# Kernel optimization log

Measured on AMD Instinct MI355X. Metric: run time of the kernel, lower is better.

## Reference

```python
import jax, jax.numpy as jnp
import numpy as np

NUM_HEADS = 8
HEAD_DIM = 64  # hidden_dim // num_heads = 512 // 8
THRESHOLD = 0.5


def setup_inputs() -> dict:
    key = jax.random.key(0)
    ks = jax.random.split(key, 12)
    B, T, D, Hd = 4, 1024, 512, 512
    s = 0.02
    inp = {
        'x': jax.random.normal(ks[0], (B, T, D), dtype=jnp.float32),
        'Wq': jax.random.normal(ks[1], (D, Hd), dtype=jnp.float32) * s,
        'bq': jnp.zeros((Hd,), jnp.float32),
        'Wk': jax.random.normal(ks[2], (D, Hd), dtype=jnp.float32) * s,
        'bk': jnp.zeros((Hd,), jnp.float32),
        'Wv': jax.random.normal(ks[3], (D, Hd), dtype=jnp.float32) * s,
        'bv': jnp.zeros((Hd,), jnp.float32),
        'conv_w': jax.random.normal(ks[4], (NUM_HEADS,), dtype=jnp.float32) * 0.3,
        'conv_b': jnp.zeros((1,), jnp.float32),
        'Wfh': jax.random.normal(ks[5], (Hd, Hd), dtype=jnp.float32) * s,
        'bfh': jnp.zeros((Hd,), jnp.float32),
        'Wfg': jax.random.normal(ks[6], (Hd, Hd), dtype=jnp.float32) * s,
        'bfg': jnp.zeros((Hd,), jnp.float32),
        'Wrh': jax.random.normal(ks[7], (Hd, Hd), dtype=jnp.float32) * s,
        'brh': jnp.zeros((Hd,), jnp.float32),
        'Wrg': jax.random.normal(ks[8], (Hd, Hd), dtype=jnp.float32) * s,
        'brg': jnp.zeros((Hd,), jnp.float32),
    }
    return inp


def reference(x, Wq, bq, Wk, bk, Wv, bv, conv_w, conv_b,
              Wfh, bfh, Wfg, bfg, Wrh, brh, Wrg, brg):
    B, T, D = x.shape
    H, hd = NUM_HEADS, HEAD_DIM
    scale = hd ** -0.5

    q = (x @ Wq + bq).reshape(B, T, H, hd).transpose(0, 2, 1, 3)  # [B,H,T,hd]
    k = (x @ Wk + bk).reshape(B, T, H, hd).transpose(0, 2, 1, 3)
    v = (x @ Wv + bv).reshape(B, T, H, hd).transpose(0, 2, 1, 3)

    scores = jnp.einsum('bhqd,bhkd->bhqk', q, k) * scale        # [B,H,T,T]
    A_t = jax.nn.softmax(scores, axis=-1)

    # cross-head 1x1 conv: weighted sum over heads -> [B,1,T,T]
    R_f = jax.nn.sigmoid(jnp.einsum('bhqk,h->bqk', A_t, conv_w) + conv_b[0])
    R_f = R_f[:, None]                                           # [B,1,T,T]
    M_f = (R_f <= THRESHOLD).astype(A_t.dtype)
    M_r = (1.0 - R_f <= THRESHOLD).astype(A_t.dtype)

    A_f = jax.nn.softmax(A_t * M_f, axis=-1)
    A_r = jax.nn.softmax(A_t * M_r, axis=-1)

    T_f = jnp.einsum('bhqk,bhkd->bhqd', A_f, v).transpose(0, 2, 1, 3).reshape(B, T, H * hd)
    T_r = jnp.einsum('bhqk,bhkd->bhqd', A_r, v).transpose(0, 2, 1, 3).reshape(B, T, H * hd)

    F_f = T_f @ Wfh + bfh
    G_f = jax.nn.sigmoid(T_f @ Wfg + bfg)
    F_r = T_r @ Wrh + brh
    G_r = jax.nn.sigmoid(T_r @ Wrg + brg)

    G_cat = jax.nn.softmax(jnp.stack([G_f, G_r], axis=-1), axis=-1)  # [B,T,Hd,2]
    F_t = F_f * G_cat[..., 0] + F_r * G_cat[..., 1]
    return F_t
```

## Files before the change

kernel.cpp:

```cpp
#include <hip/hip_runtime.h>
#include <hip/hip_bf16.h>
#include <stdint.h>

typedef short bf16x8 __attribute__((ext_vector_type(8)));
typedef float f32x4 __attribute__((ext_vector_type(4)));

__device__ __forceinline__ unsigned short f2bf(float f) {
  union { float f; unsigned int u; } v;
  v.f = f;
  unsigned int u = v.u;
  u = (u + 0x7fffu + ((u >> 16) & 1u)) >> 16;
  return (unsigned short)u;
}

__device__ __forceinline__ unsigned int pack_bf16(float x, float y) {
  return (unsigned int)f2bf(x) | ((unsigned int)f2bf(y) << 16);
}

typedef union { bf16x8 v; unsigned int u[4]; } frag_u;

__device__ __forceinline__ void gload16(const void* g, void* lds) {
  __builtin_amdgcn_global_load_lds(
      (const __attribute__((address_space(1))) unsigned int*)(unsigned long long)g,
      (__attribute__((address_space(3))) unsigned int*)(unsigned long long)(unsigned)(unsigned long long)lds,
      16, 0, 0);
}

__device__ __forceinline__ bf16x8 lds_frag(const unsigned short* t, int row, int ch4q) {
  return *(const bf16x8*)(t + row * 64 + ((ch4q ^ (row & 7)) << 3));
}


__global__ __launch_bounds__(256) void prep_kernel(
    const float* __restrict__ x,
    const float* __restrict__ Wq, const float* __restrict__ Wk, const float* __restrict__ Wv,
    const float* __restrict__ Wfh, const float* __restrict__ Wfg,
    const float* __restrict__ Wrh, const float* __restrict__ Wrg,
    unsigned short* __restrict__ xb, unsigned short* __restrict__ wt) {
  int bid = blockIdx.x;
  int tid = threadIdx.x;
  if (bid < 448) {
    __shared__ float tile[64][65];
    int mat = bid >> 6;
    int t = bid & 63;
    int tr = (t >> 3) * 64, tc = (t & 7) * 64;
    const float* W = (mat == 0) ? Wq : (mat == 1) ? Wk : (mat == 2) ? Wv
                   : (mat == 3) ? Wfh : (mat == 4) ? Wfg : (mat == 5) ? Wrh : Wrg;
    unsigned short* Wt = wt + (size_t)mat * 512 * 512;
    for (int rep = 0; rep < 16; rep++) {
      int idx = rep * 256 + tid;
      int r = idx >> 6, c = idx & 63;
      tile[r][c] = W[(tr + r) * 512 + tc + c];
    }
    __syncthreads();
    for (int rep = 0; rep < 16; rep++) {
      int idx = rep * 256 + tid;
      int r = idx >> 6, c = idx & 63;
      Wt[(tc + r) * 512 + tr + c] = f2bf(tile[c][r]);
    }
  } else {
    int blk = bid - 448;
    const float4* xi = (const float4*)x;
    for (int rep = 0; rep < 32; rep++) {
      int i = blk * 256 + tid + rep * 16384;
      float4 v = xi[i];
      unsigned int lo = (unsigned int)f2bf(v.x) | ((unsigned int)f2bf(v.y) << 16);
      unsigned int hi = (unsigned int)f2bf(v.z) | ((unsigned int)f2bf(v.w) << 16);
      uint2 u; u.x = lo; u.y = hi;
      *(uint2*)&xb[(size_t)i * 4] = u;
    }
  }
}

__global__ __launch_bounds__(256, 2) void qkv_kernel(
    const unsigned short* __restrict__ xb,
    const unsigned short* __restrict__ wtq, const unsigned short* __restrict__ wtk,
    const unsigned short* __restrict__ wtv,
    const float* __restrict__ bq, const float* __restrict__ bk, const float* __restrict__ bv,
    unsigned short* __restrict__ Qfrag, unsigned short* __restrict__ Kfrag,
    unsigned short* __restrict__ Vfrag) {
  __shared__ unsigned short As[64 * 64];
  __shared__ unsigned short Bq[64 * 64];
  __shared__ unsigned short Bk[64 * 64];
  __shared__ unsigned short Bv[64 * 64];
  __shared__ __attribute__((aligned(16))) unsigned short st[3][64 * 72];
  const int m0 = blockIdx.y * 64, n0 = blockIdx.x * 64;
  const int tid = threadIdx.x, w = tid >> 6, lane = tid & 63;
  const int c = lane & 15, quad = lane >> 4;
  const int wm = w & 1, wn = w >> 1;
  const int rsel = lane >> 3, csel = lane & 7;
  const int sc = csel ^ rsel;
  const char* Ag  = (const char*)xb  + (size_t)(m0 + w * 16 + rsel) * 1024 + sc * 16;
  const char* Bgq = (const char*)wtq + (size_t)(n0 + w * 16 + rsel) * 1024 + sc * 16;
  const char* Bgk = (const char*)wtk + (size_t)(n0 + w * 16 + rsel) * 1024 + sc * 16;
  const char* Bgv = (const char*)wtv + (size_t)(n0 + w * 16 + rsel) * 1024 + sc * 16;
  unsigned short* lA = &As[w * 1024];
  unsigned short* lQ = &Bq[w * 1024];
  unsigned short* lK = &Bk[w * 1024];
  unsigned short* lV = &Bv[w * 1024];

  f32x4 acc[3][2][2];
  f32x4 z4 = {0.f, 0.f, 0.f, 0.f};
#pragma unroll
  for (int o = 0; o < 3; o++)
#pragma unroll
    for (int i = 0; i < 2; i++)
#pragma unroll
      for (int j = 0; j < 2; j++) acc[o][i][j] = z4;

  for (int ks = 0; ks < 8; ks++) {
    if (ks) __syncthreads();
    const int kb = ks * 128;
    gload16(Ag + kb, lA);        gload16(Ag + kb + 8192, lA + 512);
    gload16(Bgq + kb, lQ);       gload16(Bgq + kb + 8192, lQ + 512);
    gload16(Bgk + kb, lK);       gload16(Bgk + kb + 8192, lK + 512);
    gload16(Bgv + kb, lV);       gload16(Bgv + kb + 8192, lV + 512);
    __syncthreads();
#pragma unroll
    for (int ch = 0; ch < 2; ch++) {
      const int cq = ch * 4 + quad;
      bf16x8 a0 = lds_frag(As, wm * 32 + c, cq);
      bf16x8 a1 = lds_frag(As, wm * 32 + 16 + c, cq);
#pragma unroll
      for (int nt = 0; nt < 2; nt++) {
        const int rb = wn * 32 + nt * 16 + c;
        bf16x8 fq = lds_frag(Bq, rb, cq);
        bf16x8 fk = lds_frag(Bk, rb, cq);
        bf16x8 fv = lds_frag(Bv, rb, cq);
        acc[0][0][nt] = __builtin_amdgcn_mfma_f32_16x16x32_bf16(a0, fq, acc[0][0][nt], 0, 0, 0);
        acc[0][1][nt] = __builtin_amdgcn_mfma_f32_16x16x32_bf16(a1, fq, acc[0][1][nt], 0, 0, 0);
        acc[1][0][nt] = __builtin_amdgcn_mfma_f32_16x16x32_bf16(a0, fk, acc[1][0][nt], 0, 0, 0);
        acc[1][1][nt] = __builtin_amdgcn_mfma_f32_16x16x32_bf16(a1, fk, acc[1][1][nt], 0, 0, 0);
        acc[2][0][nt] = __builtin_amdgcn_mfma_f32_16x16x32_bf16(a0, fv, acc[2][0][nt], 0, 0, 0);
        acc[2][1][nt] = __builtin_amdgcn_mfma_f32_16x16x32_bf16(a1, fv, acc[2][1][nt], 0, 0, 0);
      }
    }
  }

#pragma unroll
  for (int ms = 0; ms < 2; ms++)
#pragma unroll
    for (int nt = 0; nt < 2; nt++) {
      int n_l = wn * 32 + nt * 16 + c;
      int n = n0 + n_l;
      float biasq = bq[n], biask = bk[n], biasv = bv[n];
#pragma unroll
      for (int r = 0; r < 4; r++) {
        int m_l = wm * 32 + ms * 16 + quad * 4 + r;
        st[0][m_l * 72 + n_l] = f2bf((acc[0][ms][nt][r] + biasq) * 0.125f);
        st[1][m_l * 72 + n_l] = f2bf(acc[1][ms][nt][r] + biask);
        st[2][n_l * 72 + m_l] = f2bf(acc[2][ms][nt][r] + biasv);
      }
    }
  __syncthreads();

  {
    const int h = n0 >> 6;
    const int bb = m0 >> 10, t0b = (m0 & 1023) >> 4;
#pragma unroll
    for (int sub = 0; sub < 2; sub++) {
      uint4 vq = *(uint4*)&st[0][(w * 16 + c) * 72 + sub * 32 + quad * 8];
      uint4 vk = *(uint4*)&st[1][(w * 16 + c) * 72 + sub * 32 + quad * 8];
      size_t base = (size_t)((bb * 64 + t0b + w) * 8192) + h * 1024 + sub * 512 + lane * 8;
      *(uint4*)&Qfrag[base] = vq;
      *(uint4*)&Kfrag[base] = vk;
    }
    const int ktq = t0b + w;
    const int ktp = ktq >> 1, half = ktq & 1;
#pragma unroll
    for (int dm = 0; dm < 4; dm++) {
      uint2 vv = *(uint2*)&st[2][(dm * 16 + c) * 72 + w * 16 + quad * 4];
      size_t base = (size_t)(bb * 8 + h) * 65536 + (size_t)(ktp * 4 + dm) * 512
                  + lane * 8 + half * 4;
      *(uint2*)&Vfrag[base] = vv;
    }
  }
}

__global__ __launch_bounds__(512, 8) void zpass1_kernel(
    const unsigned short* __restrict__ Qfrag, const unsigned short* __restrict__ Kfrag,
    float* __restrict__ Zpart) {
  const int b = blockIdx.x >> 2, kq = blockIdx.x & 3;
  const int qt = blockIdx.y;
  const int tid = threadIdx.x, w = tid >> 6, lane = tid & 63;
  const int c = lane & 15, quad = lane >> 4;
  __shared__ float zl[8][16];
  if (tid < 128) ((float*)zl)[tid] = 0.f;
  __syncthreads();

  f32x4 z4 = {0.f, 0.f, 0.f, 0.f};
  const size_t qbase = (size_t)((b * 64 + qt) * 8192) + lane * 8;
  const int kt0 = kq * 16 + w * 2;
  const size_t kb0 = (size_t)((b * 64 + kt0) * 8192) + lane * 8;

  for (int h = 0; h < 8; h++) {
    bf16x8 qf0 = *(const bf16x8*)&Qfrag[qbase + h * 1024];
    bf16x8 qf1 = *(const bf16x8*)&Qfrag[qbase + h * 1024 + 512];
    float zh = 0.f;
#pragma unroll
    for (int i = 0; i < 2; i++) {
      const size_t kb = kb0 + (size_t)i * 8192 + h * 1024;
      bf16x8 kf0 = *(const bf16x8*)&Kfrag[kb];
      bf16x8 kf1 = *(const bf16x8*)&Kfrag[kb + 512];
      f32x4 s = __builtin_amdgcn_mfma_f32_16x16x32_bf16(kf0, qf0, z4, 0, 0, 0);
      s = __builtin_amdgcn_mfma_f32_16x16x32_bf16(kf1, qf1, s, 0, 0, 0);
      zh += __expf(s[0]) + __expf(s[1]) + __expf(s[2]) + __expf(s[3]);
    }
    zh += __shfl_xor(zh, 16); zh += __shfl_xor(zh, 32);
    if (quad == 0) atomicAdd(&zl[h][c], zh);
  }
  __syncthreads();
  if (tid < 128) {
    int h = tid >> 4, q = tid & 15;
    Zpart[(size_t)((b * 64 + qt) * 8 + h) * 64 + kq * 16 + q] = zl[h][q];
  }
}

__global__ __launch_bounds__(512, 8) void zpass2_kernel(
    const unsigned short* __restrict__ Qfrag, const unsigned short* __restrict__ Kfrag,
    const float* __restrict__ Zpart,
    const float* __restrict__ conv_w, const float* __restrict__ conv_b,
    unsigned int* __restrict__ Mfrag) {
  const int b = blockIdx.x >> 2, kq = blockIdx.x & 3;
  const int qt = blockIdx.y;
  const int tid = threadIdx.x, w = tid >> 6, lane = tid & 63;
  const int c = lane & 15;

  f32x4 z4 = {0.f, 0.f, 0.f, 0.f};
  const float cb = conv_b[0];
  const size_t qbase = (size_t)((b * 64 + qt) * 8192) + lane * 8;
  const int kt0 = kq * 16 + w * 2;
  const size_t kb0 = (size_t)((b * 64 + kt0) * 8192) + lane * 8;

  f32x4 zc0 = {cb, cb, cb, cb};
  f32x4 zc1 = zc0;

  for (int h = 0; h < 8; h++) {
    bf16x8 qf0 = *(const bf16x8*)&Qfrag[qbase + h * 1024];
    bf16x8 qf1 = *(const bf16x8*)&Qfrag[qbase + h * 1024 + 512];
    const float* zp = &Zpart[(size_t)((b * 64 + qt) * 8 + h) * 64];
    const float cwz = conv_w[h] / (zp[c] + zp[16 + c] + zp[32 + c] + zp[48 + c]);
    const size_t kba = kb0 + h * 1024;
    bf16x8 ka0 = *(const bf16x8*)&Kfrag[kba];
    bf16x8 ka1 = *(const bf16x8*)&Kfrag[kba + 512];
    bf16x8 kb0f = *(const bf16x8*)&Kfrag[kba + 8192];
    bf16x8 kb1f = *(const bf16x8*)&Kfrag[kba + 8192 + 512];
    f32x4 sa = __builtin_amdgcn_mfma_f32_16x16x32_bf16(ka0, qf0, z4, 0, 0, 0);
    sa = __builtin_amdgcn_mfma_f32_16x16x32_bf16(ka1, qf1, sa, 0, 0, 0);
    f32x4 sb = __builtin_amdgcn_mfma_f32_16x16x32_bf16(kb0f, qf0, z4, 0, 0, 0);
    sb = __builtin_amdgcn_mfma_f32_16x16x32_bf16(kb1f, qf1, sb, 0, 0, 0);
    zc0[0] += cwz * __expf(sa[0]); zc0[1] += cwz * __expf(sa[1]);
    zc0[2] += cwz * __expf(sa[2]); zc0[3] += cwz * __expf(sa[3]);
    zc1[0] += cwz * __expf(sb[0]); zc1[1] += cwz * __expf(sb[1]);
    zc1[2] += cwz * __expf(sb[2]); zc1[3] += cwz * __expf(sb[3]);
  }

  unsigned int p0 = 0, p1 = 0;
#pragma unroll
  for (int r = 0; r < 4; r++) {
    p0 |= ((zc0[r] <= 0.f ? 1u : 0u) | (zc0[r] >= 0.f ? 2u : 0u)) << (8 * r);
    p1 |= ((zc1[r] <= 0.f ? 1u : 0u) | (zc1[r] >= 0.f ? 2u : 0u)) << (8 * r);
  }
  const int ktp = kq * 8 + w;
  uint2 mm; mm.x = p0; mm.y = p1;
  *(uint2*)&Mfrag[(size_t)(b * 64 + qt) * 4096 + (size_t)ktp * 128 + lane * 2] = mm;
}

__global__ __launch_bounds__(256, 4) void pv_kernel(
    const unsigned short* __restrict__ Qfrag, const unsigned short* __restrict__ Kfrag,
    const unsigned short* __restrict__ Vfrag,
    const unsigned int* __restrict__ Mfrag, const float* __restrict__ Zpart,
    unsigned short* __restrict__ Tfb, unsigned short* __restrict__ Trb) {
  const int h = blockIdx.x;
  const int b = blockIdx.y >> 5, qb = blockIdx.y & 31;
  const int tid = threadIdx.x, w = tid >> 6, lane = tid & 63;
  const int c = lane & 15, quad = lane >> 4;
  const int qloc = w & 1, kh = w >> 1;
  const int qt = qb * 2 + qloc;

  __shared__ __attribute__((aligned(16))) float red[2][4][256][4];
  __shared__ float zb[2][2][16];

  f32x4 z4 = {0.f, 0.f, 0.f, 0.f};
  const size_t qbase = (size_t)((b * 64 + qt) * 8192) + h * 1024 + lane * 8;
  bf16x8 qf0 = *(const bf16x8*)&Qfrag[qbase];
  bf16x8 qf1 = *(const bf16x8*)&Qfrag[qbase + 512];
  const float* zpp = &Zpart[(size_t)((b * 64 + qt) * 8 + h) * 64];
  const float invZ = 1.0f / (zpp[c] + zpp[16 + c] + zpp[32 + c] + zpp[48 + c]);
  const size_t mbase = (size_t)(b * 64 + qt) * 4096 + lane * 2;
  const size_t vb0 = (size_t)(b * 8 + h) * 65536 + lane * 8;

  frag_u ones;
  ones.u[0] = 0x3F803F80u; ones.u[1] = 0x3F803F80u;
  ones.u[2] = 0x3F803F80u; ones.u[3] = 0x3F803F80u;

  f32x4 accf[4], accr[4];
#pragma unroll
  for (int i = 0; i < 4; i++) { accf[i] = z4; accr[i] = z4; }
  f32x4 acc_zf = z4, acc_zr = z4;

#pragma unroll 2
  for (int ip = 0; ip < 16; ip++) {
    const int ktp = kh * 16 + ip;
    const int kta = ktp * 2, ktb = kta + 1;
    const size_t kba = (size_t)((b * 64 + kta) * 8192) + h * 1024 + lane * 8;
    const size_t kbb = (size_t)((b * 64 + ktb) * 8192) + h * 1024 + lane * 8;
    bf16x8 ka0 = *(const bf16x8*)&Kfrag[kba];
    bf16x8 ka1 = *(const bf16x8*)&Kfrag[kba + 512];
    bf16x8 kb0 = *(const bf16x8*)&Kfrag[kbb];
    bf16x8 kb1 = *(const bf16x8*)&Kfrag[kbb + 512];
    f32x4 sa = __builtin_amdgcn_mfma_f32_16x16x32_bf16(ka0, qf0, z4, 0, 0, 0);
    sa = __builtin_amdgcn_mfma_f32_16x16x32_bf16(ka1, qf1, sa, 0, 0, 0);
    f32x4 sb = __builtin_amdgcn_mfma_f32_16x16x32_bf16(kb0, qf0, z4, 0, 0, 0);
    sb = __builtin_amdgcn_mfma_f32_16x16x32_bf16(kb1, qf1, sb, 0, 0, 0);
    const uint2 mp = *(const uint2*)&Mfrag[mbase + (size_t)ktp * 128];
    float ea[4], eb[4];
#pragma unroll
    for (int r = 0; r < 4; r++) {
      ea[r] = __expf(__expf(sa[r]) * invZ);
      eb[r] = __expf(__expf(sb[r]) * invZ);
    }
    frag_u pF, pR;
    pF.u[0] = pack_bf16((mp.x & 0x1u) ? ea[0] : 1.f, (mp.x & 0x100u) ? ea[1] : 1.f);
    pF.u[1] = pack_bf16((mp.x & 0x10000u) ? ea[2] : 1.f, (mp.x & 0x1000000u) ? ea[3] : 1.f);
    pF.u[2] = pack_bf16((mp.y & 0x1u) ? eb[0] : 1.f, (mp.y & 0x100u) ? eb[1] : 1.f);
    pF.u[3] = pack_bf16((mp.y & 0x10000u) ? eb[2] : 1.f, (mp.y & 0x1000000u) ? eb[3] : 1.f);
    pR.u[0] = pack_bf16((mp.x & 0x2u) ? ea[0] : 1.f, (mp.x & 0x200u) ? ea[1] : 1.f);
    pR.u[1] = pack_bf16((mp.x & 0x20000u) ? ea[2] : 1.f, (mp.x & 0x2000000u) ? ea[3] : 1.f);
    pR.u[2] = pack_bf16((mp.y & 0x2u) ? eb[0] : 1.f, (mp.y & 0x200u) ? eb[1] : 1.f);
    pR.u[3] = pack_bf16((mp.y & 0x20000u) ? eb[2] : 1.f, (mp.y & 0x2000000u) ? eb[3] : 1.f);
    acc_zf = __builtin_amdgcn_mfma_f32_16x16x32_bf16(ones.v, pF.v, acc_zf, 0, 0, 0);
    acc_zr = __builtin_amdgcn_mfma_f32_16x16x32_bf16(ones.v, pR.v, acc_zr, 0, 0, 0);
#pragma unroll
    for (int dm = 0; dm < 4; dm++) {
      bf16x8 vf = *(const bf16x8*)&Vfrag[vb0 + (size_t)(ktp * 4 + dm) * 512];
      accf[dm] = __builtin_amdgcn_mfma_f32_16x16x32_bf16(vf, pF.v, accf[dm], 0, 0, 0);
      accr[dm] = __builtin_amdgcn_mfma_f32_16x16x32_bf16(vf, pR.v, accr[dm], 0, 0, 0);
    }
  }

  if (kh == 1) {
#pragma unroll
    for (int dm = 0; dm < 4; dm++) *(f32x4*)red[qloc][dm][lane] = accf[dm];
    if (lane < 16) { zb[qloc][0][lane] = acc_zf[0]; zb[qloc][1][lane] = acc_zr[0]; }
  }
  __syncthreads();
  if (kh == 0) {
#pragma unroll
    for (int dm = 0; dm < 4; dm++) accf[dm] += *(f32x4*)red[qloc][dm][lane];
  }
  __syncthreads();
  if (kh == 1) {
#pragma unroll
    for (int dm = 0; dm < 4; dm++) *(f32x4*)red[qloc][dm][lane] = accr[dm];
  }
  __syncthreads();
  uint2 outf[4], outr[4];
  if (kh == 0) {
#pragma unroll
    for (int dm = 0; dm < 4; dm++) accr[dm] += *(f32x4*)red[qloc][dm][lane];
    const float zf = acc_zf[0] + zb[qloc][0][c];
    const float zr = acc_zr[0] + zb[qloc][1][c];
    const float izf = 1.0f / zf, izr = 1.0f / zr;
#pragma unroll
    for (int dm = 0; dm < 4; dm++) {
      outf[dm].x = pack_bf16(accf[dm][0] * izf, accf[dm][1] * izf);
      outf[dm].y = pack_bf16(accf[dm][2] * izf, accf[dm][3] * izf);
      outr[dm].x = pack_bf16(accr[dm][0] * izr, accr[dm][1] * izr);
      outr[dm].y = pack_bf16(accr[dm][2] * izr, accr[dm][3] * izr);
    }
  }
  __syncthreads();
  unsigned short* ts = (unsigned short*)red;
  if (kh == 0) {
    const int qrow = qloc * 16 + c;
#pragma unroll
    for (int dm = 0; dm < 4; dm++) {
      *(uint2*)&ts[qrow * 72 + dm * 16 + quad * 4] = outf[dm];
      *(uint2*)&ts[(32 + qrow) * 72 + dm * 16 + quad * 4] = outr[dm];
    }
  }
  __syncthreads();
  {
    const int row = tid >> 3, seg = tid & 7;
    const size_t g = (size_t)(b * 1024 + qb * 32 + row) * 512 + h * 64 + seg * 8;
    *(uint4*)&Tfb[g] = *(uint4*)&ts[row * 72 + seg * 8];
    *(uint4*)&Trb[g] = *(uint4*)&ts[(32 + row) * 72 + seg * 8];
  }
}

__global__ __launch_bounds__(256, 4) void final_kernel(
    const unsigned short* __restrict__ Tfb, const unsigned short* __restrict__ Trb,
    const unsigned short* __restrict__ wfh, const unsigned short* __restrict__ wfg,
    const unsigned short* __restrict__ wrh, const unsigned short* __restrict__ wrg,
    const float* __restrict__ bfh, const float* __restrict__ bfg,
    const float* __restrict__ brh, const float* __restrict__ brg,
    float* __restrict__ out) {
  __shared__ unsigned short Atf[32 * 64];
  __shared__ unsigned short Atr[32 * 64];
  __shared__ unsigned short Bfh[64 * 64];
  __shared__ unsigned short Bfg[64 * 64];
  __shared__ unsigned short Brh[64 * 64];
  __shared__ unsigned short Brg[64 * 64];
  const int m0 = blockIdx.y * 32, n0 = blockIdx.x * 64;
  const int tid = threadIdx.x, w = tid >> 6, lane = tid & 63;
  const int c = lane & 15, quad = lane >> 4;
  const int wm = w & 1, wn = w >> 1;
  const int rsel = lane >> 3, csel = lane & 7;
  const int sc = csel ^ rsel;
  const char* Agf = (const char*)Tfb + (size_t)(m0 + w * 8 + rsel) * 1024 + sc * 16;
  const char* Agr = (const char*)Trb + (size_t)(m0 + w * 8 + rsel) * 1024 + sc * 16;
  const char* Bg0 = (const char*)wfh + (size_t)(n0 + w * 16 + rsel) * 1024 + sc * 16;
  const char* Bg1 = (const char*)wfg + (size_t)(n0 + w * 16 + rsel) * 1024 + sc * 16;
  const char* Bg2 = (const char*)wrh + (size_t)(n0 + w * 16 + rsel) * 1024 + sc * 16;
  const char* Bg3 = (const char*)wrg + (size_t)(n0 + w * 16 + rsel) * 1024 + sc * 16;
  unsigned short* lAf = &Atf[w * 512];
  unsigned short* lAr = &Atr[w * 512];
  unsigned short* l0 = &Bfh[w * 1024];
  unsigned short* l1 = &Bfg[w * 1024];
  unsigned short* l2 = &Brh[w * 1024];
  unsigned short* l3 = &Brg[w * 1024];

  f32x4 acc[4][2];
  f32x4 z4 = {0.f, 0.f, 0.f, 0.f};
#pragma unroll
  for (int o = 0; o < 4; o++)
#pragma unroll
    for (int j = 0; j < 2; j++) acc[o][j] = z4;

  for (int ks = 0; ks < 8; ks++) {
    if (ks) __syncthreads();
    const int kb = ks * 128;
    gload16(Agf + kb, lAf);
    gload16(Agr + kb, lAr);
    gload16(Bg0 + kb, l0);   gload16(Bg0 + kb + 8192, l0 + 512);
    gload16(Bg1 + kb, l1);   gload16(Bg1 + kb + 8192, l1 + 512);
    gload16(Bg2 + kb, l2);   gload16(Bg2 + kb + 8192, l2 + 512);
    gload16(Bg3 + kb, l3);   gload16(Bg3 + kb + 8192, l3 + 512);
    __syncthreads();
#pragma unroll
    for (int ch = 0; ch < 2; ch++) {
      const int cq = ch * 4 + quad;
      bf16x8 af = lds_frag(Atf, wm * 16 + c, cq);
      bf16x8 ar = lds_frag(Atr, wm * 16 + c, cq);
#pragma unroll
      for (int nt = 0; nt < 2; nt++) {
        const int rb = wn * 32 + nt * 16 + c;
        bf16x8 f0 = lds_frag(Bfh, rb, cq);
        bf16x8 f1 = lds_frag(Bfg, rb, cq);
        bf16x8 f2 = lds_frag(Brh, rb, cq);
        bf16x8 f3 = lds_frag(Brg, rb, cq);
        acc[0][nt] = __builtin_amdgcn_mfma_f32_16x16x32_bf16(af, f0, acc[0][nt], 0, 0, 0);
        acc[1][nt] = __builtin_amdgcn_mfma_f32_16x16x32_bf16(af, f1, acc[1][nt], 0, 0, 0);
        acc[2][nt] = __builtin_amdgcn_mfma_f32_16x16x32_bf16(ar, f2, acc[2][nt], 0, 0, 0);
        acc[3][nt] = __builtin_amdgcn_mfma_f32_16x16x32_bf16(ar, f3, acc[3][nt], 0, 0, 0);
      }
    }
  }

#pragma unroll
  for (int nt = 0; nt < 2; nt++) {
    int n = n0 + wn * 32 + nt * 16 + c;
    float b0 = bfh[n], b1 = bfg[n], b2 = brh[n], b3 = brg[n];
    int t0 = m0 + wm * 16 + quad * 4;
#pragma unroll
    for (int r = 0; r < 4; r++) {
      int t = t0 + r;
      float Ff = acc[0][nt][r] + b0;
      float Gf = 1.0f / (1.0f + __expf(-(acc[1][nt][r] + b1)));
      float Fr = acc[2][nt][r] + b2;
      float Gr = 1.0f / (1.0f + __expf(-(acc[3][nt][r] + b3)));
      float ef = __expf(Gf), er = __expf(Gr);
      out[(size_t)t * 512 + n] = (Ff * ef + Fr * er) / (ef + er);
    }
  }
}

extern "C" void kernel_launch(void* const* d_in, const int* in_sizes, int n_in,
                              void* d_out, int out_size, void* d_ws, size_t ws_size,
                              hipStream_t stream) {
  const float* x   = (const float*)d_in[0];
  const float* Wq  = (const float*)d_in[1];
  const float* bq  = (const float*)d_in[2];
  const float* Wk  = (const float*)d_in[3];
  const float* bk  = (const float*)d_in[4];
  const float* Wv  = (const float*)d_in[5];
  const float* bv  = (const float*)d_in[6];
  const float* cw  = (const float*)d_in[7];
  const float* cb  = (const float*)d_in[8];
  const float* Wfh = (const float*)d_in[9];
  const float* bfh = (const float*)d_in[10];
  const float* Wfg = (const float*)d_in[11];
  const float* bfg = (const float*)d_in[12];
  const float* Wrh = (const float*)d_in[13];
  const float* brh = (const float*)d_in[14];
  const float* Wrg = (const float*)d_in[15];
  const float* brg = (const float*)d_in[16];

  char* ws = (char*)d_ws;
  const size_t MB = 1024 * 1024;
  unsigned short* xb    = (unsigned short*)(ws + 0 * MB);
  unsigned short* Qfrag = (unsigned short*)(ws + 4 * MB);
  unsigned short* Kfrag = (unsigned short*)(ws + 8 * MB);
  unsigned short* Vfrag = (unsigned short*)(ws + 12 * MB);
  unsigned short* Tfb   = (unsigned short*)(ws + 16 * MB);
  unsigned short* Trb   = (unsigned short*)(ws + 20 * MB);
  unsigned short* wt    = (unsigned short*)(ws + 24 * MB);
  unsigned int*   Mfrag = (unsigned int*)(ws + 28 * MB);
  float*          Zpart = (float*)(ws + 32 * MB);
  const size_t WSZ = 512 * 512;

  prep_kernel<<<512, 256, 0, stream>>>(x, Wq, Wk, Wv, Wfh, Wfg, Wrh, Wrg, xb, wt);
  qkv_kernel<<<dim3(8, 64), 256, 0, stream>>>(xb, wt + 0 * WSZ, wt + 1 * WSZ, wt + 2 * WSZ,
                                              bq, bk, bv, Qfrag, Kfrag, Vfrag);
  zpass1_kernel<<<dim3(16, 64), 512, 0, stream>>>(Qfrag, Kfrag, Zpart);
  zpass2_kernel<<<dim3(16, 64), 512, 0, stream>>>(Qfrag, Kfrag, Zpart, cw, cb, Mfrag);
  pv_kernel<<<dim3(8, 128), 256, 0, stream>>>(Qfrag, Kfrag, Vfrag, Mfrag, Zpart, Tfb, Trb);
  final_kernel<<<dim3(8, 128), 256, 0, stream>>>(Tfb, Trb, wt + 3 * WSZ, wt + 4 * WSZ,
                                                 wt + 5 * WSZ, wt + 6 * WSZ,
                                                 bfh, bfg, brh, brg, (float*)d_out);
}
```

Measured before the change: 195.4 us.

## Fuse softmax-normalizer and gate-mask passes into one kernel keeping exp scores in registers

Merges the two score passes (row-sum of exp, then cross-head gated mask) into a single kernel. Each block now covers a whole key range for one query tile, so the per-head normalizer is reduced in shared memory and the exponentials are reused from registers instead of being recomputed. It also stores the inverse normalizer directly for the PV kernel. The cost is a grid shrunk from 1024 to 256 blocks, higher register pressure from holding 8 score fragments plus gate accumulators, and two block barriers per head.

```diff
diff --git a/kernel.cpp b/kernel.cpp
--- a/kernel.cpp
+++ b/kernel.cpp
@@ -177,99 +177,76 @@
   }
 }
 
-__global__ __launch_bounds__(512, 8) void zpass1_kernel(
+__global__ __launch_bounds__(512, 4) void zgate_kernel(
     const unsigned short* __restrict__ Qfrag, const unsigned short* __restrict__ Kfrag,
-    float* __restrict__ Zpart) {
-  const int b = blockIdx.x >> 2, kq = blockIdx.x & 3;
-  const int qt = blockIdx.y;
+    const float* __restrict__ conv_w, const float* __restrict__ conv_b,
+    unsigned int* __restrict__ Mfrag, float* __restrict__ Zinv) {
+  const int b = blockIdx.x, qt = blockIdx.y;
   const int tid = threadIdx.x, w = tid >> 6, lane = tid & 63;
   const int c = lane & 15, quad = lane >> 4;
-  __shared__ float zl[8][16];
-  if (tid < 128) ((float*)zl)[tid] = 0.f;
-  __syncthreads();
+  __shared__ float zbuf[8][16];
 
   f32x4 z4 = {0.f, 0.f, 0.f, 0.f};
+  const float cb = conv_b[0];
   const size_t qbase = (size_t)((b * 64 + qt) * 8192) + lane * 8;
-  const int kt0 = kq * 16 + w * 2;
+  const int kt0 = w * 8;
   const size_t kb0 = (size_t)((b * 64 + kt0) * 8192) + lane * 8;
+
+  f32x4 g[8];
+#pragma unroll
+  for (int j = 0; j < 8; j++) g[j] = {cb, cb, cb, cb};
 
   for (int h = 0; h < 8; h++) {
     bf16x8 qf0 = *(const bf16x8*)&Qfrag[qbase + h * 1024];
     bf16x8 qf1 = *(const bf16x8*)&Qfrag[qbase + h * 1024 + 512];
+    f32x4 p[8];
     float zh = 0.f;
 #pragma unroll
-    for (int i = 0; i < 2; i++) {
-      const size_t kb = kb0 + (size_t)i * 8192 + h * 1024;
+    for (int j = 0; j < 8; j++) {
+      const size_t kb = kb0 + (size_t)j * 8192 + h * 1024;
       bf16x8 kf0 = *(const bf16x8*)&Kfrag[kb];
       bf16x8 kf1 = *(const bf16x8*)&Kfrag[kb + 512];
       f32x4 s = __builtin_amdgcn_mfma_f32_16x16x32_bf16(kf0, qf0, z4, 0, 0, 0);
       s = __builtin_amdgcn_mfma_f32_16x16x32_bf16(kf1, qf1, s, 0, 0, 0);
-      zh += __expf(s[0]) + __expf(s[1]) + __expf(s[2]) + __expf(s[3]);
+      p[j][0] = __expf(s[0]); p[j][1] = __expf(s[1]);
+      p[j][2] = __expf(s[2]); p[j][3] = __expf(s[3]);
+      zh += (p[j][0] + p[j][1]) + (p[j][2] + p[j][3]);
     }
     zh += __shfl_xor(zh, 16); zh += __shfl_xor(zh, 32);
-    if (quad == 0) atomicAdd(&zl[h][c], zh);
-  }
-  __syncthreads();
-  if (tid < 128) {
-    int h = tid >> 4, q = tid & 15;
-    Zpart[(size_t)((b * 64 + qt) * 8 + h) * 64 + kq * 16 + q] = zl[h][q];
-  }
-}
-
-__global__ __launch_bounds__(512, 8) void zpass2_kernel(
-    const unsigned short* __restrict__ Qfrag, const unsigned short* __restrict__ Kfrag,
-    const float* __restrict__ Zpart,
-    const float* __restrict__ conv_w, const float* __restrict__ conv_b,
-    unsigned int* __restrict__ Mfrag) {
-  const int b = blockIdx.x >> 2, kq = blockIdx.x & 3;
-  const int qt = blockIdx.y;
-  const int tid = threadIdx.x, w = tid >> 6, lane = tid & 63;
-  const int c = lane & 15;
-
-  f32x4 z4 = {0.f, 0.f, 0.f, 0.f};
-  const float cb = conv_b[0];
-  const size_t qbase = (size_t)((b * 64 + qt) * 8192) + lane * 8;
-  const int kt0 = kq * 16 + w * 2;
-  const size_t kb0 = (size_t)((b * 64 + kt0) * 8192) + lane * 8;
-
-  f32x4 zc0 = {cb, cb, cb, cb};
-  f32x4 zc1 = zc0;
-
-  for (int h = 0; h < 8; h++) {
-    bf16x8 qf0 = *(const bf16x8*)&Qfrag[qbase + h * 1024];
-    bf16x8 qf1 = *(const bf16x8*)&Qfrag[qbase + h * 1024 + 512];
-    const float* zp = &Zpart[(size_t)((b * 64 + qt) * 8 + h) * 64];
-    const float cwz = conv_w[h] / (zp[c] + zp[16 + c] + zp[32 + c] + zp[48 + c]);
-    const size_t kba = kb0 + h * 1024;
-    bf16x8 ka0 = *(const bf16x8*)&Kfrag[kba];
-    bf16x8 ka1 = *(const bf16x8*)&Kfrag[kba + 512];
-    bf16x8 kb0f = *(const bf16x8*)&Kfrag[kba + 8192];
-    bf16x8 kb1f = *(const bf16x8*)&Kfrag[kba + 8192 + 512];
-    f32x4 sa = __builtin_amdgcn_mfma_f32_16x16x32_bf16(ka0, qf0, z4, 0, 0, 0);
-    sa = __builtin_amdgcn_mfma_f32_16x16x32_bf16(ka1, qf1, sa, 0, 0, 0);
-    f32x4 sb = __builtin_amdgcn_mfma_f32_16x16x32_bf16(kb0f, qf0, z4, 0, 0, 0);
-    sb = __builtin_amdgcn_mfma_f32_16x16x32_bf16(kb1f, qf1, sb, 0, 0, 0);
-    zc0[0] += cwz * __expf(sa[0]); zc0[1] += cwz * __expf(sa[1]);
-    zc0[2] += cwz * __expf(sa[2]); zc0[3] += cwz * __expf(sa[3]);
-    zc1[0] += cwz * __expf(sb[0]); zc1[1] += cwz * __expf(sb[1]);
-    zc1[2] += cwz * __expf(sb[2]); zc1[3] += cwz * __expf(sb[3]);
-  }
-
-  unsigned int p0 = 0, p1 = 0;
-#pragma unroll
-  for (int r = 0; r < 4; r++) {
-    p0 |= ((zc0[r] <= 0.f ? 1u : 0u) | (zc0[r] >= 0.f ? 2u : 0u)) << (8 * r);
-    p1 |= ((zc1[r] <= 0.f ? 1u : 0u) | (zc1[r] >= 0.f ? 2u : 0u)) << (8 * r);
-  }
-  const int ktp = kq * 8 + w;
-  uint2 mm; mm.x = p0; mm.y = p1;
-  *(uint2*)&Mfrag[(size_t)(b * 64 + qt) * 4096 + (size_t)ktp * 128 + lane * 2] = mm;
+    __syncthreads();
+    if (quad == 0) zbuf[w][c] = zh;
+    __syncthreads();
+    float Z = ((zbuf[0][c] + zbuf[1][c]) + (zbuf[2][c] + zbuf[3][c]))
+            + ((zbuf[4][c] + zbuf[5][c]) + (zbuf[6][c] + zbuf[7][c]));
+    const float izq = 1.0f / Z;
+    const float cwz = conv_w[h] * izq;
+    if (w == 0 && quad == 0)
+      Zinv[(size_t)((b * 64 + qt) * 8 + h) * 16 + c] = izq;
+#pragma unroll
+    for (int j = 0; j < 8; j++) {
+      g[j][0] += cwz * p[j][0]; g[j][1] += cwz * p[j][1];
+      g[j][2] += cwz * p[j][2]; g[j][3] += cwz * p[j][3];
+    }
+  }
+
+#pragma unroll
+  for (int j = 0; j < 4; j++) {
+    unsigned int p0 = 0, p1 = 0;
+#pragma unroll
+    for (int r = 0; r < 4; r++) {
+      p0 |= ((g[2 * j][r] <= 0.f ? 1u : 0u) | (g[2 * j][r] >= 0.f ? 2u : 0u)) << (8 * r);
+      p1 |= ((g[2 * j + 1][r] <= 0.f ? 1u : 0u) | (g[2 * j + 1][r] >= 0.f ? 2u : 0u)) << (8 * r);
+    }
+    const int ktp = w * 4 + j;
+    uint2 mm; mm.x = p0; mm.y = p1;
+    *(uint2*)&Mfrag[(size_t)(b * 64 + qt) * 4096 + (size_t)ktp * 128 + lane * 2] = mm;
+  }
 }
 
 __global__ __launch_bounds__(256, 4) void pv_kernel(
     const unsigned short* __restrict__ Qfrag, const unsigned short* __restrict__ Kfrag,
     const unsigned short* __restrict__ Vfrag,
-    const unsigned int* __restrict__ Mfrag, const float* __restrict__ Zpart,
+    const unsigned int* __restrict__ Mfrag, const float* __restrict__ Zinv,
     unsigned short* __restrict__ Tfb, unsigned short* __restrict__ Trb) {
   const int h = blockIdx.x;
   const int b = blockIdx.y >> 5, qb = blockIdx.y & 31;
@@ -285,8 +262,7 @@
   const size_t qbase = (size_t)((b * 64 + qt) * 8192) + h * 1024 + lane * 8;
   bf16x8 qf0 = *(const bf16x8*)&Qfrag[qbase];
   bf16x8 qf1 = *(const bf16x8*)&Qfrag[qbase + 512];
-  const float* zpp = &Zpart[(size_t)((b * 64 + qt) * 8 + h) * 64];
-  const float invZ = 1.0f / (zpp[c] + zpp[16 + c] + zpp[32 + c] + zpp[48 + c]);
+  const float invZ = Zinv[(size_t)((b * 64 + qt) * 8 + h) * 16 + c];
   const size_t mbase = (size_t)(b * 64 + qt) * 4096 + lane * 2;
   const size_t vb0 = (size_t)(b * 8 + h) * 65536 + lane * 8;
 
@@ -507,15 +483,14 @@
   unsigned short* Trb   = (unsigned short*)(ws + 20 * MB);
   unsigned short* wt    = (unsigned short*)(ws + 24 * MB);
   unsigned int*   Mfrag = (unsigned int*)(ws + 28 * MB);
-  float*          Zpart = (float*)(ws + 32 * MB);
+  float*          Zinv  = (float*)(ws + 32 * MB);
   const size_t WSZ = 512 * 512;
 
   prep_kernel<<<512, 256, 0, stream>>>(x, Wq, Wk, Wv, Wfh, Wfg, Wrh, Wrg, xb, wt);
   qkv_kernel<<<dim3(8, 64), 256, 0, stream>>>(xb, wt + 0 * WSZ, wt + 1 * WSZ, wt + 2 * WSZ,
                                               bq, bk, bv, Qfrag, Kfrag, Vfrag);
-  zpass1_kernel<<<dim3(16, 64), 512, 0, stream>>>(Qfrag, Kfrag, Zpart);
-  zpass2_kernel<<<dim3(16, 64), 512, 0, stream>>>(Qfrag, Kfrag, Zpart, cw, cb, Mfrag);
-  pv_kernel<<<dim3(8, 128), 256, 0, stream>>>(Qfrag, Kfrag, Vfrag, Mfrag, Zpart, Tfb, Trb);
+  zgate_kernel<<<dim3(4, 64), 512, 0, stream>>>(Qfrag, Kfrag, cw, cb, Mfrag, Zinv);
+  pv_kernel<<<dim3(8, 128), 256, 0, stream>>>(Qfrag, Kfrag, Vfrag, Mfrag, Zinv, Tfb, Trb);
   final_kernel<<<dim3(8, 128), 256, 0, stream>>>(Tfb, Trb, wt + 3 * WSZ, wt + 4 * WSZ,
                                                  wt + 5 * WSZ, wt + 6 * WSZ,
                                                  bfh, bfg, brh, brg, (float*)d_out);
```

Measured after the change: 179.9 us. 7.9% less time.
